# Optimization experiments

Measured on AMD Instinct MI355X. Metric: run time of the kernel, lower is better.

The kernel has to match this reference:

```python
import jax, jax.numpy as jnp
import numpy as np

B, N, F = 256, 131072, 8


def setup_inputs() -> dict:
    key = jax.random.key(0)
    k1, k2 = jax.random.split(key)
    x = jax.random.normal(k1, (B, N), dtype=jnp.float32)
    # keras 'random_normal' initializer uses stddev=0.05; also keeps the IIR stable
    w = jax.random.normal(k2, (F,), dtype=jnp.float32) * 0.05
    return {"x": x, "w": w}


def reference(x, w):
    # Causal IIR recurrence:
    #   v[i] = 0                                   for i < F
    #   v[i] = x[i] + sum_{j=0}^{F-1} w[j] * v[i-j-1]   for i >= F
    # carry[:, j] holds v[i-1-j] for each batch row.
    Bx, Nx = x.shape
    Fw = w.shape[0]

    def step(carry, inp):
        xt, active = inp                      # xt: [B], active: scalar bool
        v = jnp.where(active, xt + carry @ w, jnp.zeros_like(xt))  # [B]
        new_carry = jnp.concatenate([v[:, None], carry[:, :-1]], axis=1)
        return new_carry, v

    carry0 = jnp.zeros((Bx, Fw), dtype=x.dtype)
    active = jnp.arange(Nx) >= Fw            # v[i]=0 until i >= filter_size
    _, ys = jax.lax.scan(step, carry0, (x.T, active))  # ys: [N, B]
    return ys.T                               # [B, N]
```

## Files before the change

### kernel.cpp

```cpp
#include <hip/hip_runtime.h>


constexpr int Bn   = 256;
constexpr int Nn   = 131072;
constexpr int Lc   = 16;
constexpr int Kn   = 32;
constexpr int TPB  = 256;
constexpr int SPAN = TPB * Lc;
constexpr int TROW = Nn / SPAN;
constexpr int PAD  = 20;

typedef float f32x4 __attribute__((ext_vector_type(4)));

#define IIR_STEP(vv, xx, a0,a1,a2,a3,a4,a5,a6,a7)                             \
    vv = fmaf(w0,(a0), fmaf(w1,(a1), fmaf(w2,(a2), fmaf(w3,(a3),              \
         fmaf(w4,(a4), fmaf(w5,(a5), fmaf(w6,(a6), fmaf(w7,(a7), (xx)))))))))

#define IIR_GROUP8(xa, xb)                                                    \
    IIR_STEP(v0, (xa).x, s0,s1,s2,s3,s4,s5,s6,s7);                            \
    IIR_STEP(v1, (xa).y, v0,s0,s1,s2,s3,s4,s5,s6);                            \
    IIR_STEP(v2, (xa).z, v1,v0,s0,s1,s2,s3,s4,s5);                            \
    IIR_STEP(v3, (xa).w, v2,v1,v0,s0,s1,s2,s3,s4);                            \
    IIR_STEP(v4, (xb).x, v3,v2,v1,v0,s0,s1,s2,s3);                            \
    IIR_STEP(v5, (xb).y, v4,v3,v2,v1,v0,s0,s1,s2);                            \
    IIR_STEP(v6, (xb).z, v5,v4,v3,v2,v1,v0,s0,s1);                            \
    IIR_STEP(v7, (xb).w, v6,v5,v4,v3,v2,v1,v0,s0);                            \
    s0=v7; s1=v6; s2=v5; s3=v4; s4=v3; s5=v2; s6=v1; s7=v0;

__global__ __launch_bounds__(256, 8)
void iir_kernel(const float* __restrict__ x,
                const float* __restrict__ wp,
                float* __restrict__ out) {
    __shared__ float tile[TPB * PAD];

    const int t    = threadIdx.x;
    const int wid  = t >> 6;
    const int lane = t & 63;
    const int b = blockIdx.x;
    const size_t base = (size_t)b * SPAN;
    const bool row_start = ((b & (TROW - 1)) == 0);

    const float w0 = wp[0], w1 = wp[1], w2 = wp[2], w3 = wp[3],
                w4 = wp[4], w5 = wp[5], w6 = wp[6], w7 = wp[7];

    float s0=0.f,s1=0.f,s2=0.f,s3=0.f,s4=0.f,s5=0.f,s6=0.f,s7=0.f;
    const int p = t * Lc;
    float* waveTile = &tile[wid * 64 * PAD];
    float* lp = &waveTile[lane * PAD];

    if (!row_start || t >= 3) {
        const float* g = x + base + p - Kn;
        const float4 a0 = *reinterpret_cast<const float4*>(g);
        const float4 a1 = *reinterpret_cast<const float4*>(g + 4);
        const float4 a2 = *reinterpret_cast<const float4*>(g + 8);
        const float4 a3 = *reinterpret_cast<const float4*>(g + 12);
        const float4 a4 = *reinterpret_cast<const float4*>(g + 16);
        const float4 a5 = *reinterpret_cast<const float4*>(g + 20);
        const float4 a6 = *reinterpret_cast<const float4*>(g + 24);
        const float4 a7 = *reinterpret_cast<const float4*>(g + 28);
        { float v0,v1,v2,v3,v4,v5,v6,v7; IIR_GROUP8(a0, a1); }
        { float v0,v1,v2,v3,v4,v5,v6,v7; IIR_GROUP8(a2, a3); }
        { float v0,v1,v2,v3,v4,v5,v6,v7; IIR_GROUP8(a4, a5); }
        { float v0,v1,v2,v3,v4,v5,v6,v7; IIR_GROUP8(a6, a7); }
        const float4 b0 = *reinterpret_cast<const float4*>(g + 32);
        const float4 b1 = *reinterpret_cast<const float4*>(g + 36);
        const float4 b2 = *reinterpret_cast<const float4*>(g + 40);
        const float4 b3 = *reinterpret_cast<const float4*>(g + 44);
        {
            float v0,v1,v2,v3,v4,v5,v6,v7;
            IIR_GROUP8(b0, b1);
            *reinterpret_cast<float4*>(lp)     = make_float4(v0,v1,v2,v3);
            *reinterpret_cast<float4*>(lp + 4) = make_float4(v4,v5,v6,v7);
        }
        {
            float v0,v1,v2,v3,v4,v5,v6,v7;
            IIR_GROUP8(b2, b3);
            *reinterpret_cast<float4*>(lp + 8)  = make_float4(v0,v1,v2,v3);
            *reinterpret_cast<float4*>(lp + 12) = make_float4(v4,v5,v6,v7);
        }
    } else if (t == 0) {
        const float* g = x + base;
        *reinterpret_cast<float4*>(lp)     = make_float4(0.f,0.f,0.f,0.f);
        *reinterpret_cast<float4*>(lp + 4) = make_float4(0.f,0.f,0.f,0.f);
        float4 xa = *reinterpret_cast<const float4*>(g + 8);
        float4 xb = *reinterpret_cast<const float4*>(g + 12);
        float v0,v1,v2,v3,v4,v5,v6,v7;
        IIR_GROUP8(xa, xb);
        *reinterpret_cast<float4*>(lp + 8)  = make_float4(v0,v1,v2,v3);
        *reinterpret_cast<float4*>(lp + 12) = make_float4(v4,v5,v6,v7);
    } else {
        const float* g = x + base;
        for (int e = 8; e < p; e += 8) {
            float4 xa = *reinterpret_cast<const float4*>(g + e);
            float4 xb = *reinterpret_cast<const float4*>(g + e + 4);
            float v0,v1,v2,v3,v4,v5,v6,v7;
            IIR_GROUP8(xa, xb);
        }
        {
            float4 xa = *reinterpret_cast<const float4*>(g + p);
            float4 xb = *reinterpret_cast<const float4*>(g + p + 4);
            float v0,v1,v2,v3,v4,v5,v6,v7;
            IIR_GROUP8(xa, xb);
            *reinterpret_cast<float4*>(lp)     = make_float4(v0,v1,v2,v3);
            *reinterpret_cast<float4*>(lp + 4) = make_float4(v4,v5,v6,v7);
        }
        {
            float4 xa = *reinterpret_cast<const float4*>(g + p + 8);
            float4 xb = *reinterpret_cast<const float4*>(g + p + 12);
            float v0,v1,v2,v3,v4,v5,v6,v7;
            IIR_GROUP8(xa, xb);
            *reinterpret_cast<float4*>(lp + 8)  = make_float4(v0,v1,v2,v3);
            *reinterpret_cast<float4*>(lp + 12) = make_float4(v4,v5,v6,v7);
        }
    }

    __threadfence_block();

    float* gout = out + base + (size_t)wid * 1024;
    #pragma unroll
    for (int k = 0; k < 4; ++k) {
        const int f   = k * 64 + lane;
        const int c   = f >> 2;
        const int off = (f & 3) * 4;
        const f32x4 v = *reinterpret_cast<const f32x4*>(&waveTile[c * PAD + off]);
        __builtin_nontemporal_store(v, reinterpret_cast<f32x4*>(gout + 4 * (size_t)f));
    }
}

extern "C" void kernel_launch(void* const* d_in, const int* in_sizes, int n_in,
                              void* d_out, int out_size, void* d_ws, size_t ws_size,
                              hipStream_t stream) {
    const float* x = (const float*)d_in[0];
    const float* w = (const float*)d_in[1];
    float* out     = (float*)d_out;

    const int grid = (Bn * Nn) / SPAN;
    iir_kernel<<<grid, TPB, 0, stream>>>(x, w, out);
}
```

Baseline: 44.09 us.

## Double per-thread chunk to 32 elements, staging output through LDS in two halves

Each thread now produces 32 outputs instead of 16 while keeping the same 32-element warm-up prefix, so the redundant recurrence work per useful output is halved and the grid shrinks by half. The output is staged through the unchanged shared tile in two 16-element halves, each written out with strided nontemporal stores. The trade-off is more serial FMA work per thread, longer per-thread latency and half as many blocks to fill the GPU, with extra block-level fences between halves.

```diff
diff --git a/kernel.cpp b/kernel.cpp
--- a/kernel.cpp
+++ b/kernel.cpp
@@ -3,7 +3,7 @@
 
 constexpr int Bn   = 256;
 constexpr int Nn   = 131072;
-constexpr int Lc   = 16;
+constexpr int Lc   = 32;
 constexpr int Kn   = 32;
 constexpr int TPB  = 256;
 constexpr int SPAN = TPB * Lc;
@@ -27,6 +27,20 @@
     IIR_STEP(v7, (xb).w, v6,v5,v4,v3,v2,v1,v0,s0);                            \
     s0=v7; s1=v6; s2=v5; s3=v4; s4=v3; s5=v2; s6=v1; s7=v0;
 
+#define HALF_TO_LDS(lp, xa, xb, xc, xd)                                       \
+    {                                                                         \
+        float v0,v1,v2,v3,v4,v5,v6,v7;                                        \
+        IIR_GROUP8(xa, xb);                                                   \
+        *reinterpret_cast<float4*>(lp)     = make_float4(v0,v1,v2,v3);        \
+        *reinterpret_cast<float4*>((lp)+4) = make_float4(v4,v5,v6,v7);        \
+    }                                                                         \
+    {                                                                         \
+        float v0,v1,v2,v3,v4,v5,v6,v7;                                        \
+        IIR_GROUP8(xc, xd);                                                   \
+        *reinterpret_cast<float4*>((lp)+8)  = make_float4(v0,v1,v2,v3);       \
+        *reinterpret_cast<float4*>((lp)+12) = make_float4(v4,v5,v6,v7);       \
+    }
+
 __global__ __launch_bounds__(256, 8)
 void iir_kernel(const float* __restrict__ x,
                 const float* __restrict__ wp,
@@ -36,7 +50,7 @@
     const int t    = threadIdx.x;
     const int wid  = t >> 6;
     const int lane = t & 63;
-    const int b = blockIdx.x;
+    const int b    = blockIdx.x;
     const size_t base = (size_t)b * SPAN;
     const bool row_start = ((b & (TROW - 1)) == 0);
 
@@ -47,83 +61,91 @@
     const int p = t * Lc;
     float* waveTile = &tile[wid * 64 * PAD];
     float* lp = &waveTile[lane * PAD];
+    const float* g = x + base + p;
 
-    if (!row_start || t >= 3) {
-        const float* g = x + base + p - Kn;
-        const float4 a0 = *reinterpret_cast<const float4*>(g);
-        const float4 a1 = *reinterpret_cast<const float4*>(g + 4);
-        const float4 a2 = *reinterpret_cast<const float4*>(g + 8);
-        const float4 a3 = *reinterpret_cast<const float4*>(g + 12);
-        const float4 a4 = *reinterpret_cast<const float4*>(g + 16);
-        const float4 a5 = *reinterpret_cast<const float4*>(g + 20);
-        const float4 a6 = *reinterpret_cast<const float4*>(g + 24);
-        const float4 a7 = *reinterpret_cast<const float4*>(g + 28);
+    if (!row_start || t >= 2) {
+        const float4 a0 = *reinterpret_cast<const float4*>(g - 32);
+        const float4 a1 = *reinterpret_cast<const float4*>(g - 28);
+        const float4 a2 = *reinterpret_cast<const float4*>(g - 24);
+        const float4 a3 = *reinterpret_cast<const float4*>(g - 20);
+        const float4 a4 = *reinterpret_cast<const float4*>(g - 16);
+        const float4 a5 = *reinterpret_cast<const float4*>(g - 12);
+        const float4 a6 = *reinterpret_cast<const float4*>(g - 8);
+        const float4 a7 = *reinterpret_cast<const float4*>(g - 4);
         { float v0,v1,v2,v3,v4,v5,v6,v7; IIR_GROUP8(a0, a1); }
         { float v0,v1,v2,v3,v4,v5,v6,v7; IIR_GROUP8(a2, a3); }
         { float v0,v1,v2,v3,v4,v5,v6,v7; IIR_GROUP8(a4, a5); }
         { float v0,v1,v2,v3,v4,v5,v6,v7; IIR_GROUP8(a6, a7); }
-        const float4 b0 = *reinterpret_cast<const float4*>(g + 32);
-        const float4 b1 = *reinterpret_cast<const float4*>(g + 36);
-        const float4 b2 = *reinterpret_cast<const float4*>(g + 40);
-        const float4 b3 = *reinterpret_cast<const float4*>(g + 44);
-        {
-            float v0,v1,v2,v3,v4,v5,v6,v7;
-            IIR_GROUP8(b0, b1);
-            *reinterpret_cast<float4*>(lp)     = make_float4(v0,v1,v2,v3);
-            *reinterpret_cast<float4*>(lp + 4) = make_float4(v4,v5,v6,v7);
-        }
-        {
-            float v0,v1,v2,v3,v4,v5,v6,v7;
-            IIR_GROUP8(b2, b3);
-            *reinterpret_cast<float4*>(lp + 8)  = make_float4(v0,v1,v2,v3);
-            *reinterpret_cast<float4*>(lp + 12) = make_float4(v4,v5,v6,v7);
-        }
+        const float4 b0 = *reinterpret_cast<const float4*>(g);
+        const float4 b1 = *reinterpret_cast<const float4*>(g + 4);
+        const float4 b2 = *reinterpret_cast<const float4*>(g + 8);
+        const float4 b3 = *reinterpret_cast<const float4*>(g + 12);
+        HALF_TO_LDS(lp, b0, b1, b2, b3);
     } else if (t == 0) {
-        const float* g = x + base;
         *reinterpret_cast<float4*>(lp)     = make_float4(0.f,0.f,0.f,0.f);
         *reinterpret_cast<float4*>(lp + 4) = make_float4(0.f,0.f,0.f,0.f);
-        float4 xa = *reinterpret_cast<const float4*>(g + 8);
-        float4 xb = *reinterpret_cast<const float4*>(g + 12);
+        const float4 b2 = *reinterpret_cast<const float4*>(g + 8);
+        const float4 b3 = *reinterpret_cast<const float4*>(g + 12);
         float v0,v1,v2,v3,v4,v5,v6,v7;
-        IIR_GROUP8(xa, xb);
+        IIR_GROUP8(b2, b3);
         *reinterpret_cast<float4*>(lp + 8)  = make_float4(v0,v1,v2,v3);
         *reinterpret_cast<float4*>(lp + 12) = make_float4(v4,v5,v6,v7);
     } else {
-        const float* g = x + base;
-        for (int e = 8; e < p; e += 8) {
-            float4 xa = *reinterpret_cast<const float4*>(g + e);
-            float4 xb = *reinterpret_cast<const float4*>(g + e + 4);
+        const float* gw = x + base;
+        for (int e = 8; e < 32; e += 8) {
+            float4 xa = *reinterpret_cast<const float4*>(gw + e);
+            float4 xb = *reinterpret_cast<const float4*>(gw + e + 4);
             float v0,v1,v2,v3,v4,v5,v6,v7;
             IIR_GROUP8(xa, xb);
         }
-        {
-            float4 xa = *reinterpret_cast<const float4*>(g + p);
-            float4 xb = *reinterpret_cast<const float4*>(g + p + 4);
-            float v0,v1,v2,v3,v4,v5,v6,v7;
-            IIR_GROUP8(xa, xb);
-            *reinterpret_cast<float4*>(lp)     = make_float4(v0,v1,v2,v3);
-            *reinterpret_cast<float4*>(lp + 4) = make_float4(v4,v5,v6,v7);
-        }
-        {
-            float4 xa = *reinterpret_cast<const float4*>(g + p + 8);
-            float4 xb = *reinterpret_cast<const float4*>(g + p + 12);
-            float v0,v1,v2,v3,v4,v5,v6,v7;
-            IIR_GROUP8(xa, xb);
-            *reinterpret_cast<float4*>(lp + 8)  = make_float4(v0,v1,v2,v3);
-            *reinterpret_cast<float4*>(lp + 12) = make_float4(v4,v5,v6,v7);
+        const float4 b0 = *reinterpret_cast<const float4*>(g);
+        const float4 b1 = *reinterpret_cast<const float4*>(g + 4);
+        const float4 b2 = *reinterpret_cast<const float4*>(g + 8);
+        const float4 b3 = *reinterpret_cast<const float4*>(g + 12);
+        HALF_TO_LDS(lp, b0, b1, b2, b3);
+    }
+
+    const float4 c0 = *reinterpret_cast<const float4*>(g + 16);
+    const float4 c1 = *reinterpret_cast<const float4*>(g + 20);
+    const float4 c2 = *reinterpret_cast<const float4*>(g + 24);
+    const float4 c3 = *reinterpret_cast<const float4*>(g + 28);
+
+    __threadfence_block();
+
+    {
+        float* gout = out + base + (size_t)wid * 2048;
+        #pragma unroll
+        for (int k = 0; k < 4; ++k) {
+            const int f   = k * 64 + lane;
+            const int c   = f >> 2;
+            const int off = (f & 3) * 4;
+            const f32x4 v = *reinterpret_cast<const f32x4*>(&waveTile[c * PAD + off]);
+            __builtin_nontemporal_store(v,
+                reinterpret_cast<f32x4*>(gout + (size_t)c * 32 + off));
         }
     }
 
     __threadfence_block();
 
-    float* gout = out + base + (size_t)wid * 1024;
-    #pragma unroll
-    for (int k = 0; k < 4; ++k) {
-        const int f   = k * 64 + lane;
-        const int c   = f >> 2;
-        const int off = (f & 3) * 4;
-        const f32x4 v = *reinterpret_cast<const f32x4*>(&waveTile[c * PAD + off]);
-        __builtin_nontemporal_store(v, reinterpret_cast<f32x4*>(gout + 4 * (size_t)f));
+    if (row_start && t == 0) {
+        HALF_TO_LDS(lp, c0, c1, c2, c3);
+    } else {
+        HALF_TO_LDS(lp, c0, c1, c2, c3);
+    }
+
+    __threadfence_block();
+
+    {
+        float* gout = out + base + (size_t)wid * 2048 + 16;
+        #pragma unroll
+        for (int k = 0; k < 4; ++k) {
+            const int f   = k * 64 + lane;
+            const int c   = f >> 2;
+            const int off = (f & 3) * 4;
+            const f32x4 v = *reinterpret_cast<const f32x4*>(&waveTile[c * PAD + off]);
+            __builtin_nontemporal_store(v,
+                reinterpret_cast<f32x4*>(gout + (size_t)c * 32 + off));
+        }
     }
 }
 
```

Measured after the change: 53.97 us. +22.4%, slower.
